# Performance work log

Measured on AMD Instinct MI355X. Metric: run time of the kernel, lower is better.

Reference implementation:

```python
import jax, jax.numpy as jnp
import numpy as np
import math

# ---------- helpers ----------

def conv(x, w, b=None, pad=1):
    y = jax.lax.conv_general_dilated(x, w, (1, 1), [(pad, pad), (pad, pad)],
                                     dimension_numbers=('NCHW', 'OIHW', 'NCHW'))
    return y if b is None else y + b[None, :, None, None]


def bn(x, g, b, m, v, eps=1e-5):
    scale = (g / jnp.sqrt(v + eps))[None, :, None, None]
    return (x - m[None, :, None, None]) * scale + b[None, :, None, None]


def _interp(x, axis, out_size):
    # bilinear resize along one axis with align_corners=True semantics
    n = x.shape[axis]
    c = jnp.arange(out_size, dtype=jnp.float32) * (n - 1) / (out_size - 1)
    lo = jnp.floor(c).astype(jnp.int32)
    hi = jnp.minimum(lo + 1, n - 1)
    w = c - lo
    xl = jnp.take(x, lo, axis=axis)
    xh = jnp.take(x, hi, axis=axis)
    wshape = [1] * x.ndim
    wshape[axis] = out_size
    w = w.reshape(wshape)
    return xl * (1.0 - w) + xh * w


def upsample2x(x):
    B, C, H, W = x.shape
    return _interp(_interp(x, 2, 2 * H), 3, 2 * W)


def haar_dwt2d(x):
    # single-level orthonormal haar DWT; equivalent to the per-(b,c) dwt2d loop,
    # vectorized over batch and channel via strided slicing
    a = x[..., 0::2, 0::2]
    b = x[..., 0::2, 1::2]
    c = x[..., 1::2, 0::2]
    d = x[..., 1::2, 1::2]
    LL = (a + b + c + d) * 0.5
    LH = (-a - b + c + d) * 0.5  # horizontal detail (row differences)
    HL = (-a + b - c + d) * 0.5  # vertical detail (col differences)
    HH = (a - b - c + d) * 0.5
    return LL, LH, HL, HH


def gabor_kernels(k=7, sigma=4.0, lambd=10.0, gamma=0.5, psi=0.0):
    thetas = jnp.array([0.0, math.pi / 4, math.pi / 2, 3 * math.pi / 4], dtype=jnp.float32)
    r = jnp.arange(-(k // 2), k // 2 + 1, dtype=jnp.float32)
    y, x = jnp.meshgrid(r, r, indexing='ij')

    def one(theta):
        xt = x * jnp.cos(theta) + y * jnp.sin(theta)
        yt = -x * jnp.sin(theta) + y * jnp.cos(theta)
        return jnp.exp(-0.5 * (xt ** 2 / sigma ** 2 + yt ** 2 / (sigma / gamma) ** 2)) \
               * jnp.cos(2.0 * math.pi * xt / lambd + psi)

    return jax.vmap(one)(thetas)[:, None]  # [4,1,k,k]


def cbam(x, fc1_w, fc2_w, sp_w):
    avg = x.mean(axis=(2, 3))
    mx = x.max(axis=(2, 3))
    mlp = lambda v: jax.nn.relu(v @ fc1_w.T) @ fc2_w.T
    ca = jax.nn.sigmoid(mlp(avg) + mlp(mx))[:, :, None, None]
    x = x * ca
    sp = jnp.concatenate([x.mean(axis=1, keepdims=True), x.max(axis=1, keepdims=True)], axis=1)
    sa = jax.nn.sigmoid(conv(sp, sp_w, pad=3))
    return x * sa


# ---------- inputs ----------

def setup_inputs() -> dict:
    B, Cin, Cout, H, W = 16, 64, 64, 128, 128
    Cr = Cout // 16
    ks = jax.random.split(jax.random.key(0), 32)
    p = lambda k, s, sc=0.05: jax.random.normal(k, s, dtype=jnp.float32) * sc
    g = lambda k, c: 1.0 + 0.1 * jax.random.normal(k, (c,), dtype=jnp.float32)
    return {
        'x': jax.random.normal(ks[0], (B, Cin, H, W), dtype=jnp.float32),
        'conv_in_w': p(ks[1], (Cout, Cin, 3, 3)),
        'bn1_g': g(ks[2], Cout), 'bn1_b': p(ks[3], (Cout,)),
        'bn1_m': p(ks[4], (Cout,)), 'bn1_v': jax.random.uniform(ks[5], (Cout,), minval=0.5, maxval=1.5),
        'down1_w': p(ks[6], (1, Cout, 3, 3)), 'down1_b': p(ks[7], (1,)),
        'down2_w': p(ks[8], (1, Cout, 3, 3)), 'down2_b': p(ks[9], (1,)),
        'wt_w': p(ks[10], (1, 1, 3, 3)), 'wt_b': p(ks[11], (1,)),
        'edge_w': p(ks[12], (Cout, 1, 3, 3)), 'edge_b': p(ks[13], (Cout,)),
        'up_w': p(ks[14], (Cout, 2, 3, 3)),
        'bn2_g': g(ks[15], Cout), 'bn2_b': p(ks[16], (Cout,)),
        'bn2_m': p(ks[17], (Cout,)), 'bn2_v': jax.random.uniform(ks[18], (Cout,), minval=0.5, maxval=1.5),
        'combine_w': p(ks[19], (Cout, 2 * Cout, 3, 3)), 'combine_b': p(ks[20], (Cout,)),
        'cbam_fc1_w': p(ks[21], (Cr, Cout)), 'cbam_fc2_w': p(ks[22], (Cout, Cr)),
        'cbam_sp_w': p(ks[23], (1, 2, 7, 7)),
        'out_w': p(ks[24], (Cout, Cout, 3, 3)),
        'bn3_g': g(ks[25], Cout), 'bn3_b': p(ks[26], (Cout,)),
        'bn3_m': p(ks[27], (Cout,)), 'bn3_v': jax.random.uniform(ks[28], (Cout,), minval=0.5, maxval=1.5),
    }


def reference(x, conv_in_w, bn1_g, bn1_b, bn1_m, bn1_v, down1_w, down1_b,
              down2_w, down2_b, wt_w, wt_b, edge_w, edge_b, up_w,
              bn2_g, bn2_b, bn2_m, bn2_v, combine_w, combine_b,
              cbam_fc1_w, cbam_fc2_w, cbam_sp_w, out_w,
              bn3_g, bn3_b, bn3_m, bn3_v):
    x1 = jax.nn.relu(bn(conv(x, conv_in_w), bn1_g, bn1_b, bn1_m, bn1_v))   # BasicConv2d
    X = upsample2x(x1)                                                      # [B,C,2H,2W]
    x_in = conv(x1, down1_w, down1_b)                                       # [B,1,H,W]
    X_in = conv(X, down2_w, down2_b)                                        # [B,1,2H,2W]
    cA, cH, cV, cD = haar_dwt2d(X_in)                                       # [B,1,H,W] each
    edge = conv(jnp.abs(cH) + jnp.abs(cV) + jnp.abs(cD), edge_w, edge_b)    # [B,C,H,W]
    gk = gabor_kernels()                                                    # all 4 thetas in one conv
    gab = jax.nn.sigmoid(conv(x_in, gk, pad=3).mean(axis=1, keepdims=True))
    wt = conv(cA, wt_w, wt_b)
    fusion = jax.nn.relu(bn(conv(jnp.concatenate([wt, gab], axis=1), up_w),
                            bn2_g, bn2_b, bn2_m, bn2_v))
    fusion = conv(jnp.concatenate([fusion, edge * (x1 + 1.0)], axis=1), combine_w, combine_b)
    att = cbam(fusion, cbam_fc1_w, cbam_fc2_w, cbam_sp_w)
    return jax.nn.relu(bn(conv(att, out_w), bn3_g, bn3_b, bn3_m, bn3_v))
```

## Files before the change

### kernel.cpp

```cpp
#include <hip/hip_runtime.h>
#include <math.h>

#define HWc 16384
#define Wd 128
#define Hd 128

typedef __attribute__((ext_vector_type(8))) _Float16 half8;
typedef __attribute__((ext_vector_type(4))) _Float16 half4;
typedef __attribute__((ext_vector_type(4))) float f32x4;

#define GLDS16(gp, lp) __builtin_amdgcn_global_load_lds( \
    (const __attribute__((address_space(1))) void*)(gp), \
    (__attribute__((address_space(3))) void*)(lp), 16, 0, 0)

__global__ void prep_wfrag_kernel(const float* __restrict__ w,
                                  _Float16* __restrict__ wf, int cin)
{
    int total = cin * 576;
    int idx = blockIdx.x * 256 + threadIdx.x;
    if (idx >= total) return;
    int KC = cin >> 5;
    int j = idx & 7;
    int lane = (idx >> 3) & 63;
    int rest = idx >> 9;
    int ot = rest & 3;
    int rest2 = rest >> 2;
    int kc = rest2 % KC;
    int t = rest2 / KC;
    int oc = ot * 16 + (lane & 15);
    int ci = kc * 32 + ((lane >> 4) << 3) + j;
    wf[idx] = (_Float16)w[((size_t)oc * cin + ci) * 9 + t];
}

__global__ __launch_bounds__(256) void pack8_kernel(const float* __restrict__ in,
                                                    _Float16* __restrict__ outp)
{
    int idx = blockIdx.x * 256 + threadIdx.x;
    int b = idx >> 14, p = idx & 16383;
    #pragma unroll
    for (int g = 0; g < 8; g++) {
        half8 v;
        #pragma unroll
        for (int k = 0; k < 8; k++)
            v[k] = (_Float16)in[((size_t)b * 64 + g * 8 + k) * HWc + p];
        *(half8*)&outp[(((size_t)b * 8 + g) * HWc + p) * 8] = v;
    }
}

__global__ __launch_bounds__(256) void mfma_conv64_kernel(
    const _Float16* __restrict__ inp8, const _Float16* __restrict__ wf,
    const float* __restrict__ bng, const float* __restrict__ bnb,
    const float* __restrict__ bnm, const float* __restrict__ bnv,
    _Float16* __restrict__ outp8, float* __restrict__ out32)
{
    __shared__ __align__(16) _Float16 slds[20736];
    __shared__ float sc[64], sh[64];
    int tid = threadIdx.x;
    int b = blockIdx.y;
    int tileid = blockIdx.x;
    int th = tileid >> 3, tw = tileid & 7;
    int h0 = th * 16 - 1, w0 = tw * 16 - 1;
    if (tid < 64) {
        float inv = rsqrtf(bnv[tid] + 1e-5f);
        float s = bng[tid] * inv;
        sc[tid] = s;
        sh[tid] = bnb[tid] - bnm[tid] * s;
    }
    const _Float16* ib = inp8 + (size_t)b * 8 * HWc * 8;
    int wid = tid >> 6;
    bool interior = (th > 0 && th < 7 && tw > 0 && tw < 7);
    if (interior) {
        #pragma unroll
        for (int it = 0; it < 11; it++) {
            int i = tid + it * 256;
            if (i < 2592) {
                int g = i / 324;
                int rem = i - g * 324;
                int y = rem / 18, x = rem - (rem / 18) * 18;
                int p = (h0 + y) * Wd + (w0 + x);
                GLDS16(&ib[((size_t)g * HWc + p) * 8],
                       &slds[(size_t)(it * 256 + wid * 64) * 8]);
            }
        }
    } else {
        #pragma unroll
        for (int it = 0; it < 11; it++) {
            int i = tid + it * 256;
            if (i < 2592) {
                half8 hz;
                #pragma unroll
                for (int k = 0; k < 8; k++) hz[k] = (_Float16)0.f;
                *(half8*)&slds[i * 8] = hz;
            }
        }
        __syncthreads();
        #pragma unroll
        for (int it = 0; it < 11; it++) {
            int i = tid + it * 256;
            if (i < 2592) {
                int g = i / 324;
                int rem = i - g * 324;
                int y = rem / 18, x = rem - (rem / 18) * 18;
                int hh = h0 + y, ww = w0 + x;
                if (hh >= 0 && hh < Hd && ww >= 0 && ww < Wd) {
                    int p = hh * Wd + ww;
                    GLDS16(&ib[((size_t)g * HWc + p) * 8],
                           &slds[(size_t)(it * 256 + wid * 64) * 8]);
                }
            }
        }
    }
    __syncthreads();
    int lane = tid & 63;
    int lq = lane >> 4, ln = lane & 15;
    int y0 = wid * 4;
    f32x4 acc[4][4];
    #pragma unroll
    for (int r = 0; r < 4; r++)
        #pragma unroll
        for (int ot = 0; ot < 4; ot++)
            #pragma unroll
            for (int q = 0; q < 4; q++) acc[r][ot][q] = 0.f;

    for (int t = 0; t < 9; t++) {
        int dy = t / 3, dx = t - (t / 3) * 3;
        #pragma unroll
        for (int kc = 0; kc < 2; kc++) {
            half8 bf[4];
            #pragma unroll
            for (int r = 0; r < 4; r++) {
                int off = (((kc * 4 + lq) * 324) + (y0 + r + dy) * 18 + (ln + dx)) * 8;
                bf[r] = *(const half8*)&slds[off];
            }
            #pragma unroll
            for (int ot = 0; ot < 4; ot++) {
                half8 af = *(const half8*)(wf + (size_t)(((t * 2 + kc) * 4 + ot) * 64 + lane) * 8);
                #pragma unroll
                for (int r = 0; r < 4; r++)
                    acc[r][ot] = __builtin_amdgcn_mfma_f32_16x16x32_f16(af, bf[r], acc[r][ot], 0, 0, 0);
            }
        }
    }
    #pragma unroll
    for (int r = 0; r < 4; r++) {
        int yy = th * 16 + y0 + r;
        int p = yy * Wd + tw * 16 + ln;
        #pragma unroll
        for (int ot = 0; ot < 4; ot++) {
            int g4 = ot * 4 + lq;
            if (out32) {
                #pragma unroll
                for (int reg = 0; reg < 4; reg++) {
                    int oc = g4 * 4 + reg;
                    float v = fmaf(acc[r][ot][reg], sc[oc], sh[oc]);
                    out32[((size_t)b * 64 + oc) * HWc + p] = fmaxf(v, 0.f);
                }
            } else {
                half4 hv;
                #pragma unroll
                for (int reg = 0; reg < 4; reg++) {
                    int oc = g4 * 4 + reg;
                    float v = fmaf(acc[r][ot][reg], sc[oc], sh[oc]);
                    hv[reg] = (_Float16)fmaxf(v, 0.f);
                }
                *(half4*)&outp8[(((size_t)b * 8 + (g4 >> 1)) * HWc + p) * 8 + (g4 & 1) * 4] = hv;
            }
        }
    }
}

__global__ __launch_bounds__(256) void mfma_combine_kernel(
    const _Float16* __restrict__ f1p, const _Float16* __restrict__ emod,
    const _Float16* __restrict__ wf, const float* __restrict__ cb,
    _Float16* __restrict__ outp8)
{
    __shared__ __align__(16) _Float16 slds[20736];
    __shared__ float cbl[64];
    int tid = threadIdx.x;
    int b = blockIdx.y;
    int tileid = blockIdx.x;
    int th = tileid >> 3, tw = tileid & 7;
    int h0 = th * 16 - 1, w0 = tw * 16 - 1;
    if (tid < 64) cbl[tid] = cb[tid];
    int wid = tid >> 6;
    int lane = tid & 63;
    int lq = lane >> 4, ln = lane & 15;
    int y0 = wid * 4;
    bool interior = (th > 0 && th < 7 && tw > 0 && tw < 7);
    f32x4 acc[4][4];
    #pragma unroll
    for (int r = 0; r < 4; r++)
        #pragma unroll
        for (int ot = 0; ot < 4; ot++)
            #pragma unroll
            for (int q = 0; q < 4; q++) acc[r][ot][q] = 0.f;

    const _Float16* f1b = f1p + (size_t)b * 8 * HWc * 8;
    const _Float16* emb = emod + (size_t)b * 8 * HWc * 8;
    for (int h = 0; h < 2; h++) {
        const _Float16* src = (h == 0) ? f1b : emb;
        if (h) __syncthreads();
        if (interior) {
            #pragma unroll
            for (int it = 0; it < 11; it++) {
                int i = tid + it * 256;
                if (i < 2592) {
                    int g = i / 324;
                    int rem = i - g * 324;
                    int y = rem / 18, x = rem - (rem / 18) * 18;
                    int p = (h0 + y) * Wd + (w0 + x);
                    GLDS16(&src[((size_t)g * HWc + p) * 8],
                           &slds[(size_t)(it * 256 + wid * 64) * 8]);
                }
            }
        } else {
            #pragma unroll
            for (int it = 0; it < 11; it++) {
                int i = tid + it * 256;
                if (i < 2592) {
                    half8 hz;
                    #pragma unroll
                    for (int k = 0; k < 8; k++) hz[k] = (_Float16)0.f;
                    *(half8*)&slds[i * 8] = hz;
                }
            }
            __syncthreads();
            #pragma unroll
            for (int it = 0; it < 11; it++) {
                int i = tid + it * 256;
                if (i < 2592) {
                    int g = i / 324;
                    int rem = i - g * 324;
                    int y = rem / 18, x = rem - (rem / 18) * 18;
                    int hh = h0 + y, ww = w0 + x;
                    if (hh >= 0 && hh < Hd && ww >= 0 && ww < Wd) {
                        int p = hh * Wd + ww;
                        GLDS16(&src[((size_t)g * HWc + p) * 8],
                               &slds[(size_t)(it * 256 + wid * 64) * 8]);
                    }
                }
            }
        }
        __syncthreads();
        for (int t = 0; t < 9; t++) {
            int dy = t / 3, dx = t - (t / 3) * 3;
            #pragma unroll
            for (int kc = 0; kc < 2; kc++) {
                int kcg = h * 2 + kc;
                half8 bf[4];
                #pragma unroll
                for (int r = 0; r < 4; r++) {
                    int off = (((kc * 4 + lq) * 324) + (y0 + r + dy) * 18 + (ln + dx)) * 8;
                    bf[r] = *(const half8*)&slds[off];
                }
                #pragma unroll
                for (int ot = 0; ot < 4; ot++) {
                    half8 af = *(const half8*)(wf + (size_t)(((t * 4 + kcg) * 4 + ot) * 64 + lane) * 8);
                    #pragma unroll
                    for (int r = 0; r < 4; r++)
                        acc[r][ot] = __builtin_amdgcn_mfma_f32_16x16x32_f16(af, bf[r], acc[r][ot], 0, 0, 0);
                }
            }
        }
    }
    #pragma unroll
    for (int r = 0; r < 4; r++) {
        int yy = th * 16 + y0 + r;
        int p = yy * Wd + tw * 16 + ln;
        #pragma unroll
        for (int ot = 0; ot < 4; ot++) {
            int g4 = ot * 4 + lq;
            half4 hv;
            #pragma unroll
            for (int reg = 0; reg < 4; reg++) {
                int oc = g4 * 4 + reg;
                hv[reg] = (_Float16)(acc[r][ot][reg] + cbl[oc]);
            }
            *(half4*)&outp8[(((size_t)b * 8 + (g4 >> 1)) * HWc + p) * 8 + (g4 & 1) * 4] = hv;
        }
    }
}

__global__ __launch_bounds__(256) void edgemul_kernel(const float* __restrict__ E,
    const _Float16* __restrict__ x1p, const float* __restrict__ edge_w,
    const float* __restrict__ edge_b, _Float16* __restrict__ emod)
{
    __shared__ float ew[576];
    __shared__ float ebl[64];
    int tid = threadIdx.x;
    for (int i = tid; i < 576; i += 256) ew[i] = edge_w[i];
    if (tid < 64) ebl[tid] = edge_b[tid];
    __syncthreads();
    int idx = blockIdx.x * 256 + tid;
    int b = idx >> 14, p = idx & 16383;
    int i = p >> 7, j = p & 127;
    const float* ep = E + (size_t)b * HWc;
    float e[9];
    #pragma unroll
    for (int tt = 0; tt < 9; tt++) {
        int ii = i - 1 + tt / 3, jj = j - 1 + tt % 3;
        e[tt] = (ii >= 0 && ii < Hd && jj >= 0 && jj < Wd) ? ep[ii * Wd + jj] : 0.f;
    }
    const _Float16* xb = x1p + (size_t)b * 8 * HWc * 8;
    _Float16* ob = emod + (size_t)b * 8 * HWc * 8;
    for (int g = 0; g < 8; g++) {
        half8 v = *(const half8*)&xb[((size_t)g * HWc + p) * 8];
        half8 hv;
        #pragma unroll
        for (int k = 0; k < 8; k++) {
            int cc = g * 8 + k;
            float ec = ebl[cc];
            #pragma unroll
            for (int tt = 0; tt < 9; tt++) ec = fmaf(ew[cc * 9 + tt], e[tt], ec);
            float xv = (float)v[k];
            hv[k] = (_Float16)(ec * (xv + 1.0f));
        }
        *(half8*)&ob[((size_t)g * HWc + p) * 8] = hv;
    }
}

__global__ __launch_bounds__(256) void modmul_kernel(const _Float16* __restrict__ fp8,
    const float* __restrict__ ca, const float* __restrict__ sa,
    _Float16* __restrict__ outm)
{
    int idx = blockIdx.x * 256 + threadIdx.x;
    int b = idx >> 14, p = idx & 16383;
    float m = sa[(size_t)b * HWc + p];
    const float* cp = ca + b * 64;
    const _Float16* fb = fp8 + (size_t)b * 8 * HWc * 8;
    _Float16* ob = outm + (size_t)b * 8 * HWc * 8;
    for (int g = 0; g < 8; g++) {
        half8 v = *(const half8*)&fb[((size_t)g * HWc + p) * 8];
        half8 hv;
        #pragma unroll
        for (int k = 0; k < 8; k++)
            hv[k] = (_Float16)((float)v[k] * cp[g * 8 + k] * m);
        *(half8*)&ob[((size_t)g * HWc + p) * 8] = hv;
    }
}

__global__ __launch_bounds__(256) void conv3x3_bn_kernel(
    const float* __restrict__ in, const float* __restrict__ wgt,
    const float* __restrict__ bng, const float* __restrict__ bnb,
    const float* __restrict__ bnm, const float* __restrict__ bnv,
    _Float16* __restrict__ outp8, int cin)
{
    __shared__ float tile[18*18];
    __shared__ float wl[576];
    __shared__ float sc[64], sh[64];
    int tid = threadIdx.x;
    int tileid = blockIdx.x; int b = blockIdx.y;
    int th = tileid >> 3, tw = tileid & 7;
    int h0 = th*16 - 1, w0 = tw*16 - 1;
    if (tid < 64) {
        float inv = rsqrtf(bnv[tid] + 1e-5f);
        float s = bng[tid]*inv;
        sc[tid] = s;
        sh[tid] = bnb[tid] - bnm[tid]*s;
    }
    float acc[64];
    #pragma unroll
    for (int i=0;i<64;i++) acc[i]=0.f;
    int py = tid>>4, px = tid&15;
    for (int ci=0; ci<cin; ci++){
        __syncthreads();
        const float* inp = in + ((size_t)b*cin + ci)*HWc;
        for (int i = tid; i < 324; i += 256) {
            int y=i/18, x=i%18; int hh=h0+y, ww=w0+x;
            tile[i] = (hh>=0&&hh<Hd&&ww>=0&&ww<Wd) ? inp[hh*Wd+ww] : 0.f;
        }
        for (int i = tid; i < 576; i += 256) {
            int oc = i/9, t = i - oc*9;
            wl[i] = wgt[((size_t)oc*cin + ci)*9 + t];
        }
        __syncthreads();
        float v[9];
        #pragma unroll
        for (int dy=0;dy<3;dy++)
            #pragma unroll
            for (int dx=0;dx<3;dx++)
                v[dy*3+dx] = tile[(py+dy)*18 + px+dx];
        #pragma unroll
        for (int oc=0;oc<64;oc++){
            float a = acc[oc];
            #pragma unroll
            for (int t=0;t<9;t++) a = fmaf(wl[oc*9+t], v[t], a);
            acc[oc]=a;
        }
    }
    int hh = h0+1+py, ww = w0+1+px;
    int p = hh*Wd + ww;
    #pragma unroll
    for (int g=0; g<8; g++){
        half8 hv;
        #pragma unroll
        for (int k=0; k<8; k++){
            int oc = g*8+k;
            float y = fmaf(acc[oc], sc[oc], sh[oc]);
            hv[k] = (_Float16)fmaxf(y, 0.f);
        }
        *(half8*)&outp8[(((size_t)b*8+g)*HWc + p)*8] = hv;
    }
}

__global__ __launch_bounds__(256) void zmaps_kernel(const _Float16* __restrict__ x1p,
    const float* __restrict__ w2, const float* __restrict__ w1,
    float* __restrict__ z, float* __restrict__ z1)
{
    int idx = blockIdx.x*256 + threadIdx.x;
    int b = idx >> 14; int p = idx & 16383;
    const _Float16* xb = x1p + (size_t)b*8*HWc*8;
    float a2[9], a1[9];
    #pragma unroll
    for (int t=0;t<9;t++){ a2[t]=0.f; a1[t]=0.f; }
    for (int g=0; g<8; g++){
        half8 v = *(const half8*)&xb[((size_t)g*HWc + p)*8];
        #pragma unroll
        for (int k=0;k<8;k++){
            int c = g*8+k;
            float val = (float)v[k];
            #pragma unroll
            for (int t=0;t<9;t++){
                a2[t] = fmaf(w2[c*9+t], val, a2[t]);
                a1[t] = fmaf(w1[c*9+t], val, a1[t]);
            }
        }
    }
    #pragma unroll
    for (int t=0;t<9;t++){
        z [((size_t)b*9+t)*HWc + p] = a2[t];
        z1[((size_t)b*9+t)*HWc + p] = a1[t];
    }
}

__global__ __launch_bounds__(256) void xin_kernel(const float* __restrict__ z1,
    const float* __restrict__ b1p, float* __restrict__ xin)
{
    int idx = blockIdx.x*256+threadIdx.x;
    int b=idx>>14; int p=idx&16383;
    int i=p>>7, j=p&127;
    float acc = b1p[0];
    #pragma unroll
    for (int t=0;t<9;t++){
        int ii=i+t/3-1, jj=j+t%3-1;
        if (ii>=0&&ii<Hd&&jj>=0&&jj<Wd)
            acc += z1[((size_t)b*9+t)*HWc + ii*Wd+jj];
    }
    xin[idx]=acc;
}

__global__ __launch_bounds__(256) void dwt_kernel(const float* __restrict__ z,
    const float* __restrict__ b2p, float* __restrict__ cA, float* __restrict__ Eo)
{
    int idx = blockIdx.x*256 + threadIdx.x;
    int b = idx >> 14; int p = idx & 16383;
    int u = p >> 7, v = p & 127;
    float b2 = b2p[0];
    int rlo[4], rhi[4]; float rf[4]; bool rv[4];
    int clo[4], chi[4]; float cf[4]; bool cvv[4];
    #pragma unroll
    for (int k=0;k<4;k++){
        int r = 2*u - 1 + k;
        rv[k] = (r>=0 && r<256);
        int rr = rv[k] ? r : 0;
        float cc = ((float)rr * 127.0f) / 255.0f;
        int lo = (int)cc;
        rlo[k]=lo; rhi[k]=min(lo+1,127); rf[k]=cc-(float)lo;
        int s = 2*v - 1 + k;
        cvv[k] = (s>=0 && s<256);
        int ss = cvv[k] ? s : 0;
        float c2 = ((float)ss * 127.0f) / 255.0f;
        int lo2=(int)c2;
        clo[k]=lo2; chi[k]=min(lo2+1,127); cf[k]=c2-(float)lo2;
    }
    float Xin[4] = {b2,b2,b2,b2};
    #pragma unroll
    for (int t=0;t<9;t++){
        int dy=t/3, dx=t%3;
        const float* zp = z + ((size_t)b*9 + t)*HWc;
        #pragma unroll
        for (int e=0;e<4;e++){
            int ey=e>>1, ex=e&1;
            int k=ey+dy, l=ex+dx;
            if (rv[k] && cvv[l]){
                const float* row0 = zp + rlo[k]*Wd;
                const float* row1 = zp + rhi[k]*Wd;
                float v00=row0[clo[l]], v01=row0[chi[l]];
                float v10=row1[clo[l]], v11=row1[chi[l]];
                float fc_=cf[l], fr_=rf[k];
                float top = v00*(1.0f-fc_) + v01*fc_;
                float bot = v10*(1.0f-fc_) + v11*fc_;
                Xin[e] += top*(1.0f-fr_) + bot*fr_;
            }
        }
    }
    float a=Xin[0], bb=Xin[1], c_=Xin[2], d_=Xin[3];
    float LL=0.5f*( a+bb+c_+d_);
    float LH=0.5f*(-a-bb+c_+d_);
    float HL=0.5f*(-a+bb-c_+d_);
    float HH=0.5f*( a-bb-c_+d_);
    cA[(size_t)b*HWc + p] = LL;
    Eo[(size_t)b*HWc + p] = fabsf(LH)+fabsf(HL)+fabsf(HH);
}

__global__ __launch_bounds__(256) void wtgab_kernel(const float* __restrict__ cA,
    const float* __restrict__ xin, const float* __restrict__ wtw, const float* __restrict__ wtb,
    float* __restrict__ wtgab)
{
    __shared__ float gm[49];
    int tid=threadIdx.x;
    if (tid<49){
        int ky=tid/7, kx=tid%7;
        float yy=(float)(ky-3), xx=(float)(kx-3);
        float s=0.f;
        for (int t=0;t<4;t++){
            float theta = (float)t * 0.7853981633974483f;
            float ct=cosf(theta), st=sinf(theta);
            float xt = xx*ct + yy*st;
            float yt = -xx*st + yy*ct;
            s += expf(-0.5f*(xt*xt*(1.0f/16.0f) + yt*yt*(1.0f/64.0f))) * cosf(0.6283185307179586f*xt);
        }
        gm[tid]=0.25f*s;
    }
    __syncthreads();
    int idx = blockIdx.x*256+tid;
    int b=idx>>14; int p=idx&16383;
    int i=p>>7, j=p&127;
    float wacc = wtb[0];
    #pragma unroll
    for (int t=0;t<9;t++){
        int ii=i+t/3-1, jj=j+t%3-1;
        if (ii>=0&&ii<Hd&&jj>=0&&jj<Wd)
            wacc = fmaf(wtw[t], cA[b*HWc + ii*Wd+jj], wacc);
    }
    float g=0.f;
    for (int k=0;k<49;k++){
        int ii=i+k/7-3, jj=j+k%7-3;
        if (ii>=0&&ii<Hd&&jj>=0&&jj<Wd)
            g = fmaf(gm[k], xin[b*HWc + ii*Wd+jj], g);
    }
    wtgab[((size_t)b*2)*HWc + p] = wacc;
    wtgab[((size_t)b*2+1)*HWc + p] = 1.0f/(1.0f+expf(-g));
}

__global__ __launch_bounds__(256) void pool_kernel(const _Float16* __restrict__ fp8,
    float* __restrict__ pavg, float* __restrict__ pmax)
{
    int b = blockIdx.x >> 3, g = blockIdx.x & 7;
    int tid = threadIdx.x;
    const _Float16* p = fp8 + ((size_t)b*8 + g)*HWc*8;
    float s[8] = {0,0,0,0,0,0,0,0};
    float m[8] = {-3.4e38f,-3.4e38f,-3.4e38f,-3.4e38f,-3.4e38f,-3.4e38f,-3.4e38f,-3.4e38f};
    for (int i=tid;i<HWc;i+=256){
        half8 v = *(const half8*)&p[(size_t)i*8];
        #pragma unroll
        for (int k=0;k<8;k++){ float u=(float)v[k]; s[k]+=u; m[k]=fmaxf(m[k],u); }
    }
    __shared__ float ss[8][256], sm[8][256];
    #pragma unroll
    for (int k=0;k<8;k++){ ss[k][tid]=s[k]; sm[k][tid]=m[k]; }
    __syncthreads();
    for (int st=128; st>0; st>>=1){
        if (tid<st){
            #pragma unroll
            for (int k=0;k<8;k++){
                ss[k][tid]+=ss[k][tid+st];
                sm[k][tid]=fmaxf(sm[k][tid],sm[k][tid+st]);
            }
        }
        __syncthreads();
    }
    if (tid<8){
        pavg[b*64 + g*8 + tid] = ss[tid][0]*(1.0f/16384.0f);
        pmax[b*64 + g*8 + tid] = sm[tid][0];
    }
}

__global__ void mlp_kernel(const float* __restrict__ pavg, const float* __restrict__ pmax,
    const float* __restrict__ fc1, const float* __restrict__ fc2, float* __restrict__ ca)
{
    int b = blockIdx.x; int tid = threadIdx.x;
    __shared__ float hs[4];
    if (tid < 4){
        float sa_=0.f, sm_=0.f;
        for (int c=0;c<64;c++){
            float w = fc1[tid*64+c];
            sa_ = fmaf(w, pavg[b*64+c], sa_);
            sm_ = fmaf(w, pmax[b*64+c], sm_);
        }
        hs[tid] = fmaxf(sa_,0.f) + fmaxf(sm_,0.f);
    }
    __syncthreads();
    float o = 0.f;
    #pragma unroll
    for (int j=0;j<4;j++) o = fmaf(fc2[tid*4+j], hs[j], o);
    ca[b*64+tid] = 1.0f/(1.0f+expf(-o));
}

__global__ __launch_bounds__(256) void spstats_kernel(const _Float16* __restrict__ fp8,
    const float* __restrict__ ca, float* __restrict__ spmean, float* __restrict__ spmax)
{
    int idx = blockIdx.x*256+threadIdx.x;
    int b = idx>>14; int p = idx&16383;
    const _Float16* fb = fp8 + (size_t)b*8*HWc*8;
    const float* cp = ca + b*64;
    float s=0.f, m=-3.4e38f;
    for (int g=0; g<8; g++){
        half8 v = *(const half8*)&fb[((size_t)g*HWc + p)*8];
        #pragma unroll
        for (int k=0;k<8;k++){
            float u = (float)v[k] * cp[g*8+k];
            s += u; m = fmaxf(m, u);
        }
    }
    spmean[idx] = s*(1.0f/64.0f);
    spmax[idx] = m;
}

__global__ __launch_bounds__(256) void spconv_kernel(const float* __restrict__ spmean,
    const float* __restrict__ spmax, const float* __restrict__ spw, float* __restrict__ sa)
{
    int idx = blockIdx.x*256+threadIdx.x;
    int b=idx>>14; int p=idx&16383;
    int i=p>>7, j=p&127;
    float acc=0.f;
    for (int k=0;k<49;k++){
        int ky=k/7-3, kx=k%7-3;
        int ii=i+ky, jj=j+kx;
        if (ii>=0&&ii<Hd&&jj>=0&&jj<Wd){
            int q = b*HWc + ii*Wd+jj;
            acc = fmaf(spw[k],    spmean[q], acc);
            acc = fmaf(spw[49+k], spmax[q], acc);
        }
    }
    sa[idx] = 1.0f/(1.0f+expf(-acc));
}

extern "C" void kernel_launch(void* const* d_in, const int* in_sizes, int n_in,
                              void* d_out, int out_size, void* d_ws, size_t ws_size,
                              hipStream_t stream)
{
    const float* x         = (const float*)d_in[0];
    const float* conv_in_w = (const float*)d_in[1];
    const float* bn1_g = (const float*)d_in[2];
    const float* bn1_b = (const float*)d_in[3];
    const float* bn1_m = (const float*)d_in[4];
    const float* bn1_v = (const float*)d_in[5];
    const float* down1_w = (const float*)d_in[6];
    const float* down1_b = (const float*)d_in[7];
    const float* down2_w = (const float*)d_in[8];
    const float* down2_b = (const float*)d_in[9];
    const float* wt_w = (const float*)d_in[10];
    const float* wt_b = (const float*)d_in[11];
    const float* edge_w = (const float*)d_in[12];
    const float* edge_b = (const float*)d_in[13];
    const float* up_w = (const float*)d_in[14];
    const float* bn2_g = (const float*)d_in[15];
    const float* bn2_b = (const float*)d_in[16];
    const float* bn2_m = (const float*)d_in[17];
    const float* bn2_v = (const float*)d_in[18];
    const float* combine_w = (const float*)d_in[19];
    const float* combine_b = (const float*)d_in[20];
    const float* fc1 = (const float*)d_in[21];
    const float* fc2 = (const float*)d_in[22];
    const float* spw = (const float*)d_in[23];
    const float* out_w = (const float*)d_in[24];
    const float* bn3_g = (const float*)d_in[25];
    const float* bn3_b = (const float*)d_in[26];
    const float* bn3_m = (const float*)d_in[27];
    const float* bn3_v = (const float*)d_in[28];
    float* out = (float*)d_out;
    float* ws = (float*)d_ws;

    float* z       = ws;
    float* z1      = z + 2359296;
    float* xin     = z1 + 2359296;
    float* cA      = xin + 262144;
    float* Ebuf    = cA + 262144;
    float* wtgab   = Ebuf + 262144;
    float* spmean  = wtgab + 524288;
    float* spmaxb  = spmean + 262144;
    float* sabuf   = spmaxb + 262144;
    float* pavg    = sabuf + 262144;
    float* pmaxb   = pavg + 1024;
    float* cab     = pmaxb + 1024;
    _Float16* xp      = (_Float16*)(cab + 1024);
    _Float16* x1p     = xp + 16777216;
    _Float16* f1p     = x1p + 16777216;
    _Float16* fp      = f1p + 16777216;
    _Float16* wf_in   = fp + 16777216;
    _Float16* wf_out  = wf_in + 36864;
    _Float16* wf_comb = wf_out + 36864;
    _Float16* emod = xp;
    _Float16* fmod = f1p;

    prep_wfrag_kernel<<<144, 256, 0, stream>>>(conv_in_w, wf_in, 64);
    prep_wfrag_kernel<<<144, 256, 0, stream>>>(out_w, wf_out, 64);
    prep_wfrag_kernel<<<288, 256, 0, stream>>>(combine_w, wf_comb, 128);
    pack8_kernel<<<1024, 256, 0, stream>>>(x, xp);

    dim3 cgrid(64, 16);
    mfma_conv64_kernel<<<cgrid, 256, 0, stream>>>(xp, wf_in, bn1_g,bn1_b,bn1_m,bn1_v,
                                                  x1p, nullptr);
    zmaps_kernel<<<1024, 256, 0, stream>>>(x1p, down2_w, down1_w, z, z1);
    xin_kernel<<<1024, 256, 0, stream>>>(z1, down1_b, xin);
    dwt_kernel<<<1024, 256, 0, stream>>>(z, down2_b, cA, Ebuf);
    wtgab_kernel<<<1024, 256, 0, stream>>>(cA, xin, wt_w, wt_b, wtgab);
    conv3x3_bn_kernel<<<cgrid, 256, 0, stream>>>(wtgab, up_w, bn2_g,bn2_b,bn2_m,bn2_v, f1p, 2);
    edgemul_kernel<<<1024, 256, 0, stream>>>(Ebuf, x1p, edge_w, edge_b, emod);
    mfma_combine_kernel<<<cgrid, 256, 0, stream>>>(f1p, emod, wf_comb, combine_b, fp);
    pool_kernel<<<128, 256, 0, stream>>>(fp, pavg, pmaxb);
    mlp_kernel<<<16, 64, 0, stream>>>(pavg, pmaxb, fc1, fc2, cab);
    spstats_kernel<<<1024, 256, 0, stream>>>(fp, cab, spmean, spmaxb);
    spconv_kernel<<<1024, 256, 0, stream>>>(spmean, spmaxb, spw, sabuf);
    modmul_kernel<<<1024, 256, 0, stream>>>(fp, cab, sabuf, fmod);
    mfma_conv64_kernel<<<cgrid, 256, 0, stream>>>(fmod, wf_out, bn3_g,bn3_b,bn3_m,bn3_v,
                                                  nullptr, out);
}
```

Measured before the change: 551.1 us.

## Shrink MFMA conv blocks to one wave per 4x16 tile and fuse spconv with modmul

The 64-channel MFMA conv and combine kernels now use 64-thread blocks, each covering a 4-row by 16-column tile with a 6x18 halo in LDS, in place of 256-thread blocks covering 16x16 tiles. This gives four times as many blocks and a smaller LDS footprint, for more blocks in flight and better CU fill. The cost is more halo reloading per output pixel (6 input rows per 4 output rows instead of 18 per 16). Border tiles now zero-fill only out-of-bounds halo entries, dropping the separate zeroing pass and its barrier. The spatial-attention conv is fused with the channel/spatial modulation multiply, which removes the sa buffer round trip and one launch.

Result: faster. 495.1 us (-10.2%).

```diff
diff --git a/kernel.cpp b/kernel.cpp
--- a/kernel.cpp
+++ b/kernel.cpp
@@ -47,73 +47,62 @@
     }
 }
 
-__global__ __launch_bounds__(256) void mfma_conv64_kernel(
+__global__ __launch_bounds__(64, 4) void mfma_conv64_kernel(
     const _Float16* __restrict__ inp8, const _Float16* __restrict__ wf,
     const float* __restrict__ bng, const float* __restrict__ bnb,
     const float* __restrict__ bnm, const float* __restrict__ bnv,
     _Float16* __restrict__ outp8, float* __restrict__ out32)
 {
-    __shared__ __align__(16) _Float16 slds[20736];
+    __shared__ __align__(16) _Float16 slds[6912];
     __shared__ float sc[64], sh[64];
-    int tid = threadIdx.x;
+    int lane = threadIdx.x;
     int b = blockIdx.y;
     int tileid = blockIdx.x;
-    int th = tileid >> 3, tw = tileid & 7;
-    int h0 = th * 16 - 1, w0 = tw * 16 - 1;
-    if (tid < 64) {
-        float inv = rsqrtf(bnv[tid] + 1e-5f);
-        float s = bng[tid] * inv;
-        sc[tid] = s;
-        sh[tid] = bnb[tid] - bnm[tid] * s;
+    int ty = tileid >> 3, tx = tileid & 7;
+    int h0 = ty * 4 - 1, w0 = tx * 16 - 1;
+    {
+        float inv = rsqrtf(bnv[lane] + 1e-5f);
+        float s = bng[lane] * inv;
+        sc[lane] = s;
+        sh[lane] = bnb[lane] - bnm[lane] * s;
     }
     const _Float16* ib = inp8 + (size_t)b * 8 * HWc * 8;
-    int wid = tid >> 6;
-    bool interior = (th > 0 && th < 7 && tw > 0 && tw < 7);
+    bool interior = (ty >= 1 && ty <= 30 && tx >= 1 && tx <= 6);
     if (interior) {
         #pragma unroll
-        for (int it = 0; it < 11; it++) {
-            int i = tid + it * 256;
-            if (i < 2592) {
-                int g = i / 324;
-                int rem = i - g * 324;
+        for (int it = 0; it < 14; it++) {
+            int i = it * 64 + lane;
+            if (i < 864) {
+                int g = i / 108;
+                int rem = i - g * 108;
                 int y = rem / 18, x = rem - (rem / 18) * 18;
                 int p = (h0 + y) * Wd + (w0 + x);
-                GLDS16(&ib[((size_t)g * HWc + p) * 8],
-                       &slds[(size_t)(it * 256 + wid * 64) * 8]);
+                GLDS16(&ib[((size_t)g * HWc + p) * 8], &slds[it * 512]);
             }
         }
     } else {
         #pragma unroll
-        for (int it = 0; it < 11; it++) {
-            int i = tid + it * 256;
-            if (i < 2592) {
-                half8 hz;
-                #pragma unroll
-                for (int k = 0; k < 8; k++) hz[k] = (_Float16)0.f;
-                *(half8*)&slds[i * 8] = hz;
-            }
-        }
-        __syncthreads();
-        #pragma unroll
-        for (int it = 0; it < 11; it++) {
-            int i = tid + it * 256;
-            if (i < 2592) {
-                int g = i / 324;
-                int rem = i - g * 324;
+        for (int it = 0; it < 14; it++) {
+            int i = it * 64 + lane;
+            if (i < 864) {
+                int g = i / 108;
+                int rem = i - g * 108;
                 int y = rem / 18, x = rem - (rem / 18) * 18;
                 int hh = h0 + y, ww = w0 + x;
                 if (hh >= 0 && hh < Hd && ww >= 0 && ww < Wd) {
                     int p = hh * Wd + ww;
-                    GLDS16(&ib[((size_t)g * HWc + p) * 8],
-                           &slds[(size_t)(it * 256 + wid * 64) * 8]);
+                    GLDS16(&ib[((size_t)g * HWc + p) * 8], &slds[it * 512]);
+                } else {
+                    half8 hz;
+                    #pragma unroll
+                    for (int k = 0; k < 8; k++) hz[k] = (_Float16)0.f;
+                    *(half8*)&slds[i * 8] = hz;
                 }
             }
         }
     }
     __syncthreads();
-    int lane = tid & 63;
     int lq = lane >> 4, ln = lane & 15;
-    int y0 = wid * 4;
     f32x4 acc[4][4];
     #pragma unroll
     for (int r = 0; r < 4; r++)
@@ -129,7 +118,7 @@
             half8 bf[4];
             #pragma unroll
             for (int r = 0; r < 4; r++) {
-                int off = (((kc * 4 + lq) * 324) + (y0 + r + dy) * 18 + (ln + dx)) * 8;
+                int off = (((kc * 4 + lq) * 108) + (r + dy) * 18 + (ln + dx)) * 8;
                 bf[r] = *(const half8*)&slds[off];
             }
             #pragma unroll
@@ -143,8 +132,8 @@
     }
     #pragma unroll
     for (int r = 0; r < 4; r++) {
-        int yy = th * 16 + y0 + r;
-        int p = yy * Wd + tw * 16 + ln;
+        int yy = ty * 4 + r;
+        int p = yy * Wd + tx * 16 + ln;
         #pragma unroll
         for (int ot = 0; ot < 4; ot++) {
             int g4 = ot * 4 + lq;
@@ -169,24 +158,21 @@
     }
 }
 
-__global__ __launch_bounds__(256) void mfma_combine_kernel(
+__global__ __launch_bounds__(64, 4) void mfma_combine_kernel(
     const _Float16* __restrict__ f1p, const _Float16* __restrict__ emod,
     const _Float16* __restrict__ wf, const float* __restrict__ cb,
     _Float16* __restrict__ outp8)
 {
-    __shared__ __align__(16) _Float16 slds[20736];
+    __shared__ __align__(16) _Float16 slds[6912];
     __shared__ float cbl[64];
-    int tid = threadIdx.x;
+    int lane = threadIdx.x;
     int b = blockIdx.y;
     int tileid = blockIdx.x;
-    int th = tileid >> 3, tw = tileid & 7;
-    int h0 = th * 16 - 1, w0 = tw * 16 - 1;
-    if (tid < 64) cbl[tid] = cb[tid];
-    int wid = tid >> 6;
-    int lane = tid & 63;
+    int ty = tileid >> 3, tx = tileid & 7;
+    int h0 = ty * 4 - 1, w0 = tx * 16 - 1;
+    cbl[lane] = cb[lane];
     int lq = lane >> 4, ln = lane & 15;
-    int y0 = wid * 4;
-    bool interior = (th > 0 && th < 7 && tw > 0 && tw < 7);
+    bool interior = (ty >= 1 && ty <= 30 && tx >= 1 && tx <= 6);
     f32x4 acc[4][4];
     #pragma unroll
     for (int r = 0; r < 4; r++)
@@ -202,41 +188,33 @@
         if (h) __syncthreads();
         if (interior) {
             #pragma unroll
-            for (int it = 0; it < 11; it++) {
-                int i = tid + it * 256;
-                if (i < 2592) {
-                    int g = i / 324;
-                    int rem = i - g * 324;
+            for (int it = 0; it < 14; it++) {
+                int i = it * 64 + lane;
+                if (i < 864) {
+                    int g = i / 108;
+                    int rem = i - g * 108;
                     int y = rem / 18, x = rem - (rem / 18) * 18;
                     int p = (h0 + y) * Wd + (w0 + x);
-                    GLDS16(&src[((size_t)g * HWc + p) * 8],
-                           &slds[(size_t)(it * 256 + wid * 64) * 8]);
+                    GLDS16(&src[((size_t)g * HWc + p) * 8], &slds[it * 512]);
                 }
             }
         } else {
             #pragma unroll
-            for (int it = 0; it < 11; it++) {
-                int i = tid + it * 256;
-                if (i < 2592) {
-                    half8 hz;
-                    #pragma unroll
-                    for (int k = 0; k < 8; k++) hz[k] = (_Float16)0.f;
-                    *(half8*)&slds[i * 8] = hz;
-                }
-            }
-            __syncthreads();
-            #pragma unroll
-            for (int it = 0; it < 11; it++) {
-                int i = tid + it * 256;
-                if (i < 2592) {
-                    int g = i / 324;
-                    int rem = i - g * 324;
+            for (int it = 0; it < 14; it++) {
+                int i = it * 64 + lane;
+                if (i < 864) {
+                    int g = i / 108;
+                    int rem = i - g * 108;
                     int y = rem / 18, x = rem - (rem / 18) * 18;
                     int hh = h0 + y, ww = w0 + x;
                     if (hh >= 0 && hh < Hd && ww >= 0 && ww < Wd) {
                         int p = hh * Wd + ww;
-                        GLDS16(&src[((size_t)g * HWc + p) * 8],
-                               &slds[(size_t)(it * 256 + wid * 64) * 8]);
+                        GLDS16(&src[((size_t)g * HWc + p) * 8], &slds[it * 512]);
+                    } else {
+                        half8 hz;
+                        #pragma unroll
+                        for (int k = 0; k < 8; k++) hz[k] = (_Float16)0.f;
+                        *(half8*)&slds[i * 8] = hz;
                     }
                 }
             }
@@ -250,7 +228,7 @@
                 half8 bf[4];
                 #pragma unroll
                 for (int r = 0; r < 4; r++) {
-                    int off = (((kc * 4 + lq) * 324) + (y0 + r + dy) * 18 + (ln + dx)) * 8;
+                    int off = (((kc * 4 + lq) * 108) + (r + dy) * 18 + (ln + dx)) * 8;
                     bf[r] = *(const half8*)&slds[off];
                 }
                 #pragma unroll
@@ -265,8 +243,8 @@
     }
     #pragma unroll
     for (int r = 0; r < 4; r++) {
-        int yy = th * 16 + y0 + r;
-        int p = yy * Wd + tw * 16 + ln;
+        int yy = ty * 4 + r;
+        int p = yy * Wd + tx * 16 + ln;
         #pragma unroll
         for (int ot = 0; ot < 4; ot++) {
             int g4 = ot * 4 + lq;
@@ -315,26 +293,6 @@
             float xv = (float)v[k];
             hv[k] = (_Float16)(ec * (xv + 1.0f));
         }
-        *(half8*)&ob[((size_t)g * HWc + p) * 8] = hv;
-    }
-}
-
-__global__ __launch_bounds__(256) void modmul_kernel(const _Float16* __restrict__ fp8,
-    const float* __restrict__ ca, const float* __restrict__ sa,
-    _Float16* __restrict__ outm)
-{
-    int idx = blockIdx.x * 256 + threadIdx.x;
-    int b = idx >> 14, p = idx & 16383;
-    float m = sa[(size_t)b * HWc + p];
-    const float* cp = ca + b * 64;
-    const _Float16* fb = fp8 + (size_t)b * 8 * HWc * 8;
-    _Float16* ob = outm + (size_t)b * 8 * HWc * 8;
-    for (int g = 0; g < 8; g++) {
-        half8 v = *(const half8*)&fb[((size_t)g * HWc + p) * 8];
-        half8 hv;
-        #pragma unroll
-        for (int k = 0; k < 8; k++)
-            hv[k] = (_Float16)((float)v[k] * cp[g * 8 + k] * m);
         *(half8*)&ob[((size_t)g * HWc + p) * 8] = hv;
     }
 }
@@ -617,8 +575,10 @@
     spmax[idx] = m;
 }
 
-__global__ __launch_bounds__(256) void spconv_kernel(const float* __restrict__ spmean,
-    const float* __restrict__ spmax, const float* __restrict__ spw, float* __restrict__ sa)
+__global__ __launch_bounds__(256) void spconv_modmul_kernel(
+    const float* __restrict__ spmean, const float* __restrict__ spmax,
+    const float* __restrict__ spw, const _Float16* __restrict__ fp8,
+    const float* __restrict__ ca, _Float16* __restrict__ outm)
 {
     int idx = blockIdx.x*256+threadIdx.x;
     int b=idx>>14; int p=idx&16383;
@@ -633,7 +593,18 @@
             acc = fmaf(spw[49+k], spmax[q], acc);
         }
     }
-    sa[idx] = 1.0f/(1.0f+expf(-acc));
+    float m = 1.0f/(1.0f+expf(-acc));
+    const float* cp = ca + b * 64;
+    const _Float16* fb = fp8 + (size_t)b * 8 * HWc * 8;
+    _Float16* ob = outm + (size_t)b * 8 * HWc * 8;
+    for (int g = 0; g < 8; g++) {
+        half8 v = *(const half8*)&fb[((size_t)g * HWc + p) * 8];
+        half8 hv;
+        #pragma unroll
+        for (int k = 0; k < 8; k++)
+            hv[k] = (_Float16)((float)v[k] * cp[g * 8 + k] * m);
+        *(half8*)&ob[((size_t)g * HWc + p) * 8] = hv;
+    }
 }
 
 extern "C" void kernel_launch(void* const* d_in, const int* in_sizes, int n_in,
@@ -699,21 +670,20 @@
     prep_wfrag_kernel<<<288, 256, 0, stream>>>(combine_w, wf_comb, 128);
     pack8_kernel<<<1024, 256, 0, stream>>>(x, xp);
 
-    dim3 cgrid(64, 16);
-    mfma_conv64_kernel<<<cgrid, 256, 0, stream>>>(xp, wf_in, bn1_g,bn1_b,bn1_m,bn1_v,
-                                                  x1p, nullptr);
+    dim3 cgrid(256, 16);
+    mfma_conv64_kernel<<<cgrid, 64, 0, stream>>>(xp, wf_in, bn1_g,bn1_b,bn1_m,bn1_v,
+                                                 x1p, nullptr);
     zmaps_kernel<<<1024, 256, 0, stream>>>(x1p, down2_w, down1_w, z, z1);
     xin_kernel<<<1024, 256, 0, stream>>>(z1, down1_b, xin);
     dwt_kernel<<<1024, 256, 0, stream>>>(z, down2_b, cA, Ebuf);
     wtgab_kernel<<<1024, 256, 0, stream>>>(cA, xin, wt_w, wt_b, wtgab);
-    conv3x3_bn_kernel<<<cgrid, 256, 0, stream>>>(wtgab, up_w, bn2_g,bn2_b,bn2_m,bn2_v, f1p, 2);
+    conv3x3_bn_kernel<<<dim3(64,16), 256, 0, stream>>>(wtgab, up_w, bn2_g,bn2_b,bn2_m,bn2_v, f1p, 2);
     edgemul_kernel<<<1024, 256, 0, stream>>>(Ebuf, x1p, edge_w, edge_b, emod);
-    mfma_combine_kernel<<<cgrid, 256, 0, stream>>>(f1p, emod, wf_comb, combine_b, fp);
+    mfma_combine_kernel<<<cgrid, 64, 0, stream>>>(f1p, emod, wf_comb, combine_b, fp);
     pool_kernel<<<128, 256, 0, stream>>>(fp, pavg, pmaxb);
     mlp_kernel<<<16, 64, 0, stream>>>(pavg, pmaxb, fc1, fc2, cab);
     spstats_kernel<<<1024, 256, 0, stream>>>(fp, cab, spmean, spmaxb);
-    spconv_kernel<<<1024, 256, 0, stream>>>(spmean, spmaxb, spw, sabuf);
-    modmul_kernel<<<1024, 256, 0, stream>>>(fp, cab, sabuf, fmod);
-    mfma_conv64_kernel<<<cgrid, 256, 0, stream>>>(fmod, wf_out, bn3_g,bn3_b,bn3_m,bn3_v,
-                                                  nullptr, out);
-}
+    spconv_modmul_kernel<<<1024, 256, 0, stream>>>(spmean, spmaxb, spw, fp, cab, fmod);
+    mfma_conv64_kernel<<<cgrid, 64, 0, stream>>>(fmod, wf_out, bn3_g,bn3_b,bn3_m,bn3_v,
+                                                 nullptr, out);
+}
```
